# Kernel optimization log

Hardware: AMD Instinct MI355X
Metric: run time of the kernel (lower is better)

## Reference

```python
import jax, jax.numpy as jnp
import numpy as np

ATTR_LEN = [2, 4, 4, 2, 6]
CUM = np.concatenate(([0], np.cumsum(ATTR_LEN)))  # [0,2,6,10,12,18]
B, S, D, V = 4096, 200, 64, 100000


def setup_inputs() -> dict:
    key = jax.random.key(0)
    ks = jax.random.split(key, 10)
    x = jax.random.randint(ks[0], (B, S), 0, V)
    # one-hot labels per attribute, concatenated -> [B, 18]
    y_parts = []
    for i, al in enumerate(ATTR_LEN):
        lab = jax.random.randint(jax.random.fold_in(ks[1], i), (B,), 0, al)
        y_parts.append(jax.nn.one_hot(lab, al, dtype=jnp.float32))
    y = jnp.concatenate(y_parts, axis=1)
    emb_table = jax.random.normal(ks[2], (V, D), jnp.float32) * 0.02
    emb_table = emb_table.at[0].set(0.0)  # padding_idx=0
    att_w = jax.random.normal(ks[3], (5, D), jnp.float32) * 0.1
    att_b = jax.random.normal(ks[4], (5,), jnp.float32) * 0.1
    W0 = jax.random.normal(ks[5], (ATTR_LEN[0], D), jnp.float32) * 0.1
    W1 = jax.random.normal(ks[6], (ATTR_LEN[1], D), jnp.float32) * 0.1
    W2 = jax.random.normal(ks[7], (ATTR_LEN[2], D), jnp.float32) * 0.1
    W3 = jax.random.normal(ks[8], (ATTR_LEN[3], D), jnp.float32) * 0.1
    W4 = jax.random.normal(ks[9], (ATTR_LEN[4], D), jnp.float32) * 0.1
    return {"x": x, "y": y, "emb_table": emb_table, "att_w": att_w,
            "att_b": att_b, "W0": W0, "W1": W1, "W2": W2, "W3": W3, "W4": W4}


def reference(x, y, emb_table, att_w, att_b, W0, W1, W2, W3, W4):
    embed = emb_table[x]  # [B, S, D] gather (padding row is zero)
    # 5 per-attribute additive tanh-attention heads, batched over k.
    # Softmax over seq axis is independent per head, so stacking is exact.
    att_u = jnp.tanh(jnp.einsum('bsd,kd->bsk', embed, att_w) + att_b)  # [B,S,5]
    score = jax.nn.softmax(att_u, axis=1)                              # [B,S,5]
    user_rep = jnp.einsum('bsd,bsk->bkd', embed, score)                # [B,5,D]
    Ws = [W0, W1, W2, W3, W4]
    # per-task bias-free linear heads, concatenated -> [B, 18]
    W_user = jnp.concatenate([user_rep[:, i] @ Ws[i].T for i in range(5)], axis=1)
    logits = []
    loss = jnp.float32(0.0)
    for i in range(5):
        Wc = W_user[:, CUM[i]:CUM[i + 1]]
        yc = y[:, CUM[i]:CUM[i + 1]]
        # partial_training=False -> ob = ones -> all rows kept;
        # obj = exp(sum(W*y)) / sum_j exp(W_j)  ==  softmax picked at label
        logp = jax.nn.log_softmax(Wc, axis=1)
        loss = loss + (-jnp.sum(logp * yc) / Wc.shape[0])
        logits.append(jax.nn.softmax(Wc, axis=1))
    logit = jnp.concatenate(logits, axis=1)  # [B, 18]
    return logit, loss
```

## Files before the change

### kernel.cpp

```cpp
#include <hip/hip_runtime.h>
#include <math.h>

#define Bsz 4096
#define Ssz 200
#define Dsz 64
#define NK  5
#define NT  512
#define ROWH 72

typedef _Float16 half_t;
typedef _Float16 h2 __attribute__((ext_vector_type(2)));

__device__ inline h2 shfl_xor_h2(h2 v, int m) {
    int iv = __builtin_bit_cast(int, v);
    iv = __shfl_xor(iv, m);
    return __builtin_bit_cast(h2, iv);
}

__device__ inline h2 pk(float a, float b) {
    return __builtin_bit_cast(h2, __builtin_amdgcn_cvt_pkrtz(a, b));
}

__device__ inline float fdot2(h2 a, h2 b, float c) {
#if __has_builtin(__builtin_amdgcn_fdot2)
    return __builtin_amdgcn_fdot2(a, b, c, false);
#else
    return c + (float)a.x * (float)b.x + (float)a.y * (float)b.y;
#endif
}

__device__ inline float fast_tanh(float x) {
    float e = __expf(-2.0f * fabsf(x));
    float r = (1.0f - e) / (1.0f + e);
    return copysignf(r, x);
}

__global__ void zero_loss_kernel(float* loss) {
    if (threadIdx.x == 0) *loss = 0.0f;
}

__global__ __launch_bounds__(NT, 8) void tan_kernel(
    const int* __restrict__ x, const float* __restrict__ y,
    const float* __restrict__ emb_table,
    const float* __restrict__ att_w, const float* __restrict__ att_b,
    const float* __restrict__ W0, const float* __restrict__ W1,
    const float* __restrict__ W2, const float* __restrict__ W3,
    const float* __restrict__ W4,
    float* __restrict__ out_logit, float* __restrict__ loss_out)
{
    __shared__ alignas(16) half_t embh[Ssz * ROWH];
    __shared__ alignas(16) char   ovl[8 * NK * Dsz * 2];
    __shared__ alignas(16) h2     att5[100][8];
    __shared__ alignas(16) float  ur[NK][Dsz];
    __shared__ alignas(16) h2     awh[NK * 32];
    __shared__ alignas(16) int    xs[Ssz];
    __shared__ float wu[18];

    float*  att  = (float*)ovl;
    half_t (*urph)[NK][Dsz] = (half_t(*)[NK][Dsz])ovl;

    const int b   = blockIdx.x;
    const int tid = threadIdx.x;
    const int w   = tid >> 6;
    const int l   = tid & 63;

    if (tid < Ssz) xs[tid] = x[b * Ssz + tid];
    if (tid >= 256 && tid < 256 + NK * 32) {
        const int t = tid - 256;
        awh[t] = (h2){(half_t)att_w[2 * t], (half_t)att_w[2 * t + 1]};
    }
    __syncthreads();

    {
        float4 v[7];
#pragma unroll
        for (int p = 0; p < 7; ++p) {
            int i = tid + NT * p;
            if (i > Ssz * 16 - 1) i = Ssz * 16 - 1;
            const int s = i >> 4, c = i & 15;
            v[p] = ((const float4*)(emb_table + (size_t)xs[s] * Dsz))[c];
        }
#pragma unroll
        for (int p = 0; p < 7; ++p) {
            const int i = tid + NT * p;
            if (p < 6 || i < Ssz * 16) {
                const int s = i >> 4, c = i & 15;
                h2 lo = pk(v[p].x, v[p].y);
                h2 hi = pk(v[p].z, v[p].w);
                uint2 u = { __builtin_bit_cast(unsigned, lo),
                            __builtin_bit_cast(unsigned, hi) };
                *(uint2*)(embh + s * ROWH + c * 4) = u;
            }
        }
    }
    __syncthreads();

    if (tid < 2 * Ssz) {
        const int s = tid >> 1, h = tid & 1;
        union { uint4 q[4]; h2 hh[16]; } ue;
        const uint4* rp = (const uint4*)(embh + s * ROWH + h * 32);
#pragma unroll
        for (int i = 0; i < 4; ++i) ue.q[i] = rp[i];
        float acc[NK];
#pragma unroll 1
        for (int k = 0; k < NK; ++k) {
            union { uint4 q[4]; h2 hh[16]; } ua;
            const uint4* ap = (const uint4*)(awh + k * 32 + h * 16);
#pragma unroll
            for (int i = 0; i < 4; ++i) ua.q[i] = ap[i];
            float a = 0.f;
#pragma unroll
            for (int i = 0; i < 16; ++i) a = fdot2(ue.hh[i], ua.hh[i], a);
            acc[k] = a;
        }
#pragma unroll
        for (int k = 0; k < NK; ++k) acc[k] += __shfl_xor(acc[k], 1);
        if (h == 0) {
#pragma unroll
            for (int k = 0; k < NK; ++k)
                att[k * Ssz + s] = fast_tanh(acc[k] + att_b[k]);
        }
    }
    __syncthreads();

    if (w < NK) {
        const int k = w;
        float vals[4];
        float mx = -1e30f;
#pragma unroll
        for (int j = 0; j < 4; ++j) {
            int s = l + 64 * j;
            vals[j] = (s < Ssz) ? att[k * Ssz + s] : -1e30f;
            mx = fmaxf(mx, vals[j]);
        }
#pragma unroll
        for (int m = 32; m >= 1; m >>= 1) mx = fmaxf(mx, __shfl_xor(mx, m));
        float sum = 0.f;
#pragma unroll
        for (int j = 0; j < 4; ++j) {
            vals[j] = __expf(vals[j] - mx);
            sum += vals[j];
        }
#pragma unroll
        for (int m = 32; m >= 1; m >>= 1) sum += __shfl_xor(sum, m);
        float inv = 1.0f / sum;
#pragma unroll
        for (int j = 0; j < 4; ++j) {
            const int s = l + 64 * j;
            float scv = vals[j] * inv;
            float pnr = __shfl_xor(scv, 1);
            if (s < Ssz && (l & 1) == 0)
                att5[s >> 1][k] = pk(scv, pnr);
        }
    }
    __syncthreads();

    {
        const int c = tid & 15;
        const int j = tid >> 4;
        h2 acc[NK][2];
#pragma unroll
        for (int k = 0; k < NK; ++k) {
            acc[k][0] = (h2){(half_t)0, (half_t)0};
            acc[k][1] = (h2){(half_t)0, (half_t)0};
        }
#pragma unroll
        for (int t = 0; t < 4; ++t) {
            const int p = j + 32 * t;
            if (p < 100) {
                const int s0 = 2 * p;
                union { uint2 q; h2 hh[2]; } e0, e1;
                e0.q = *(const uint2*)(embh + s0 * ROWH + c * 4);
                e1.q = *(const uint2*)(embh + (s0 + 1) * ROWH + c * 4);
                union { uint4 q; h2 hh[4]; } sq;
                sq.q = *(const uint4*)(&att5[p][0]);
                h2 s4 = att5[p][4];
#pragma unroll
                for (int k = 0; k < NK; ++k) {
                    h2 sp = (k < 4) ? sq.hh[k] : s4;
                    h2 sc0 = (h2){sp.x, sp.x};
                    h2 sc1 = (h2){sp.y, sp.y};
                    acc[k][0] += e0.hh[0] * sc0;
                    acc[k][1] += e0.hh[1] * sc0;
                    acc[k][0] += e1.hh[0] * sc1;
                    acc[k][1] += e1.hh[1] * sc1;
                }
            }
        }
#pragma unroll
        for (int k = 0; k < NK; ++k)
#pragma unroll
            for (int i = 0; i < 2; ++i) {
                acc[k][i] += shfl_xor_h2(acc[k][i], 16);
                acc[k][i] += shfl_xor_h2(acc[k][i], 32);
            }
        if (l < 16) {
#pragma unroll
            for (int k = 0; k < NK; ++k) {
                union { h2 a[2]; uint2 q; } uu;
                uu.a[0] = acc[k][0]; uu.a[1] = acc[k][1];
                *(uint2*)(&urph[w][k][l * 4]) = uu.q;
            }
        }
    }
    __syncthreads();

    if (tid < NK * Dsz) {
        const int k = tid >> 6, d = tid & 63;
        float ssum = 0.f;
#pragma unroll
        for (int jj = 0; jj < 8; ++jj) ssum += (float)urph[jj][k][d];
        ur[k][d] = ssum;
    }
    __syncthreads();

    for (int j = w; j < 18; j += 8) {
        const float* Wp; int g, c0;
        if      (j < 2)  { g = 0; c0 = 0;  Wp = W0; }
        else if (j < 6)  { g = 1; c0 = 2;  Wp = W1; }
        else if (j < 10) { g = 2; c0 = 6;  Wp = W2; }
        else if (j < 12) { g = 3; c0 = 10; Wp = W3; }
        else             { g = 4; c0 = 12; Wp = W4; }
        float p = ur[g][l] * Wp[(j - c0) * Dsz + l];
#pragma unroll
        for (int m = 32; m >= 1; m >>= 1) p += __shfl_xor(p, m);
        if (l == 0) wu[j] = p;
    }
    __syncthreads();

    if (w == 0) {
        float lossb = 0.f;
        if (l < NK) {
            const int LEN[5] = {2, 4, 4, 2, 6};
            const int C0[5]  = {0, 2, 6, 10, 12};
            const int g = l, c0 = C0[g], len = LEN[g];
            float* op = out_logit + (size_t)b * 18;
            const float* yp = y + (size_t)b * 18;
            float mx = -1e30f;
            for (int j = 0; j < len; ++j) mx = fmaxf(mx, wu[c0 + j]);
            float sum = 0.f;
            for (int j = 0; j < len; ++j) sum += __expf(wu[c0 + j] - mx);
            float inv = 1.0f / sum;
            float lse = mx + __logf(sum);
            for (int j = 0; j < len; ++j) {
                op[c0 + j] = __expf(wu[c0 + j] - mx) * inv;
                lossb += (lse - wu[c0 + j]) * yp[c0 + j];
            }
        }
#pragma unroll
        for (int m = 1; m <= 4; m <<= 1) lossb += __shfl_xor(lossb, m);
        if (l == 0) atomicAdd(loss_out, lossb * (1.0f / Bsz));
    }
}

extern "C" void kernel_launch(void* const* d_in, const int* in_sizes, int n_in,
                              void* d_out, int out_size, void* d_ws, size_t ws_size,
                              hipStream_t stream) {
    const int*   x   = (const int*)d_in[0];
    const float* y   = (const float*)d_in[1];
    const float* emb = (const float*)d_in[2];
    const float* aw  = (const float*)d_in[3];
    const float* ab  = (const float*)d_in[4];
    const float* W0  = (const float*)d_in[5];
    const float* W1  = (const float*)d_in[6];
    const float* W2  = (const float*)d_in[7];
    const float* W3  = (const float*)d_in[8];
    const float* W4  = (const float*)d_in[9];
    float* out  = (float*)d_out;
    float* loss = out + (size_t)Bsz * 18;

    zero_loss_kernel<<<1, 64, 0, stream>>>(loss);
    tan_kernel<<<Bsz, NT, 0, stream>>>(x, y, emb, aw, ab,
                                       W0, W1, W2, W3, W4, out, loss);
}
```

Measured before the change: 151.5 us.

## Use MFMA for attention scores and weighted pooling with transposed embedding copy

Replaces the scalar fdot2 score computation and the packed-half weighted-sum pooling with 16x16x32 f16 MFMA instructions. A second, transposed copy of the embeddings is written to shared memory so the pooling MFMA reads contiguous sequence-major fragments. Scores are stored as padded half arrays, and the pooled result is reduced across two wave halves in fp32. This raises shared-memory use and lowers the launch-bounds occupancy hint from 8 to 4, and the scattered scalar transposed stores may cause bank conflicts. Most MFMA lanes are wasted because only 5 heads are computed.

```diff
diff --git a/kernel.cpp b/kernel.cpp
--- a/kernel.cpp
+++ b/kernel.cpp
@@ -1,32 +1,23 @@
 #include <hip/hip_runtime.h>
 #include <math.h>
+#include <stdint.h>
 
 #define Bsz 4096
 #define Ssz 200
 #define Dsz 64
 #define NK  5
 #define NT  512
-#define ROWH 72
 
 typedef _Float16 half_t;
-typedef _Float16 h2 __attribute__((ext_vector_type(2)));
-
-__device__ inline h2 shfl_xor_h2(h2 v, int m) {
-    int iv = __builtin_bit_cast(int, v);
-    iv = __shfl_xor(iv, m);
-    return __builtin_bit_cast(h2, iv);
-}
+typedef _Float16 h2    __attribute__((ext_vector_type(2)));
+typedef _Float16 f16x8 __attribute__((ext_vector_type(8)));
+typedef float    f32x4 __attribute__((ext_vector_type(4)));
+
+#define RSTRIDE 72
+#define TSTRIDE 232
 
 __device__ inline h2 pk(float a, float b) {
     return __builtin_bit_cast(h2, __builtin_amdgcn_cvt_pkrtz(a, b));
-}
-
-__device__ inline float fdot2(h2 a, h2 b, float c) {
-#if __has_builtin(__builtin_amdgcn_fdot2)
-    return __builtin_amdgcn_fdot2(a, b, c, false);
-#else
-    return c + (float)a.x * (float)b.x + (float)a.y * (float)b.y;
-#endif
 }
 
 __device__ inline float fast_tanh(float x) {
@@ -39,7 +30,7 @@
     if (threadIdx.x == 0) *loss = 0.0f;
 }
 
-__global__ __launch_bounds__(NT, 8) void tan_kernel(
+__global__ __launch_bounds__(NT, 4) void tan_kernel(
     const int* __restrict__ x, const float* __restrict__ y,
     const float* __restrict__ emb_table,
     const float* __restrict__ att_w, const float* __restrict__ att_b,
@@ -48,26 +39,38 @@
     const float* __restrict__ W4,
     float* __restrict__ out_logit, float* __restrict__ loss_out)
 {
-    __shared__ alignas(16) half_t embh[Ssz * ROWH];
-    __shared__ alignas(16) char   ovl[8 * NK * Dsz * 2];
-    __shared__ alignas(16) h2     att5[100][8];
-    __shared__ alignas(16) float  ur[NK][Dsz];
-    __shared__ alignas(16) h2     awh[NK * 32];
+    __shared__ alignas(16) half_t embR[208 * RSTRIDE];
+    __shared__ alignas(16) half_t embT[64 * TSTRIDE];
+    __shared__ alignas(16) float  ovl[1000];
+    __shared__ alignas(16) half_t ascore[NK * 240];
+    __shared__ alignas(16) half_t awh[NK * RSTRIDE];
     __shared__ alignas(16) int    xs[Ssz];
     __shared__ float wu[18];
 
-    float*  att  = (float*)ovl;
-    half_t (*urph)[NK][Dsz] = (half_t(*)[NK][Dsz])ovl;
+    float* att_raw = ovl;
 
     const int b   = blockIdx.x;
     const int tid = threadIdx.x;
     const int w   = tid >> 6;
     const int l   = tid & 63;
+    const int col = l & 15;
+    const int kg  = l >> 4;
 
     if (tid < Ssz) xs[tid] = x[b * Ssz + tid];
+    {
+        uint4 z = {0u, 0u, 0u, 0u};
+        if (tid < 72)
+            *(uint4*)((char*)embR + 200 * 144 + tid * 16) = z;
+        if (tid >= 72 && tid < 72 + 192) {
+            const int idx = tid - 72, row = idx / 3, q = idx - row * 3;
+            *(uint4*)((char*)embT + row * 464 + 400 + q * 16) = z;
+        }
+    }
     if (tid >= 256 && tid < 256 + NK * 32) {
-        const int t = tid - 256;
-        awh[t] = (h2){(half_t)att_w[2 * t], (half_t)att_w[2 * t + 1]};
+        const int t = tid - 256, row = t >> 5, cp = t & 31;
+        h2 v = {(half_t)att_w[row * 64 + 2 * cp],
+                (half_t)att_w[row * 64 + 2 * cp + 1]};
+        *(h2*)(awh + row * RSTRIDE + 2 * cp) = v;
     }
     __syncthreads();
 
@@ -89,36 +92,36 @@
                 h2 hi = pk(v[p].z, v[p].w);
                 uint2 u = { __builtin_bit_cast(unsigned, lo),
                             __builtin_bit_cast(unsigned, hi) };
-                *(uint2*)(embh + s * ROWH + c * 4) = u;
+                *(uint2*)(embR + s * RSTRIDE + c * 4) = u;
+                embT[(4 * c + 0) * TSTRIDE + s] = lo.x;
+                embT[(4 * c + 1) * TSTRIDE + s] = lo.y;
+                embT[(4 * c + 2) * TSTRIDE + s] = hi.x;
+                embT[(4 * c + 3) * TSTRIDE + s] = hi.y;
             }
         }
     }
     __syncthreads();
 
-    if (tid < 2 * Ssz) {
-        const int s = tid >> 1, h = tid & 1;
-        union { uint4 q[4]; h2 hh[16]; } ue;
-        const uint4* rp = (const uint4*)(embh + s * ROWH + h * 32);
-#pragma unroll
-        for (int i = 0; i < 4; ++i) ue.q[i] = rp[i];
-        float acc[NK];
-#pragma unroll 1
-        for (int k = 0; k < NK; ++k) {
-            union { uint4 q[4]; h2 hh[16]; } ua;
-            const uint4* ap = (const uint4*)(awh + k * 32 + h * 16);
-#pragma unroll
-            for (int i = 0; i < 4; ++i) ua.q[i] = ap[i];
-            float a = 0.f;
-#pragma unroll
-            for (int i = 0; i < 16; ++i) a = fdot2(ue.hh[i], ua.hh[i], a);
-            acc[k] = a;
-        }
-#pragma unroll
-        for (int k = 0; k < NK; ++k) acc[k] += __shfl_xor(acc[k], 1);
-        if (h == 0) {
-#pragma unroll
-            for (int k = 0; k < NK; ++k)
-                att[k * Ssz + s] = fast_tanh(acc[k] + att_b[k]);
+    {
+        const int brow = (col < 5) ? col : 0;
+        const f16x8 bw0 = *(const f16x8*)(awh + brow * RSTRIDE + kg * 8);
+        const f16x8 bw1 = *(const f16x8*)(awh + brow * RSTRIDE + 32 + kg * 8);
+        const float bk = att_b[brow];
+        for (int t = w; t < 13; t += 8) {
+            const int s = 16 * t + col;
+            const f16x8 a0 = *(const f16x8*)(embR + s * RSTRIDE + kg * 8);
+            const f16x8 a1 = *(const f16x8*)(embR + s * RSTRIDE + 32 + kg * 8);
+            f32x4 acc = {0.f, 0.f, 0.f, 0.f};
+            acc = __builtin_amdgcn_mfma_f32_16x16x32_f16(a0, bw0, acc, 0, 0, 0);
+            acc = __builtin_amdgcn_mfma_f32_16x16x32_f16(a1, bw1, acc, 0, 0, 0);
+            if (col < 5) {
+#pragma unroll
+                for (int r = 0; r < 4; ++r) {
+                    const int srow = 16 * t + 4 * kg + r;
+                    if (srow < Ssz)
+                        att_raw[col * 200 + srow] = fast_tanh(acc[r] + bk);
+                }
+            }
         }
     }
     __syncthreads();
@@ -129,8 +132,8 @@
         float mx = -1e30f;
 #pragma unroll
         for (int j = 0; j < 4; ++j) {
-            int s = l + 64 * j;
-            vals[j] = (s < Ssz) ? att[k * Ssz + s] : -1e30f;
+            const int s = l + 64 * j;
+            vals[j] = (s < Ssz) ? att_raw[k * 200 + s] : -1e30f;
             mx = fmaxf(mx, vals[j]);
         }
 #pragma unroll
@@ -143,85 +146,49 @@
         }
 #pragma unroll
         for (int m = 32; m >= 1; m >>= 1) sum += __shfl_xor(sum, m);
-        float inv = 1.0f / sum;
+        const float inv = 1.0f / sum;
 #pragma unroll
         for (int j = 0; j < 4; ++j) {
             const int s = l + 64 * j;
-            float scv = vals[j] * inv;
-            float pnr = __shfl_xor(scv, 1);
-            if (s < Ssz && (l & 1) == 0)
-                att5[s >> 1][k] = pk(scv, pnr);
-        }
-    }
-    __syncthreads();
-
-    {
-        const int c = tid & 15;
-        const int j = tid >> 4;
-        h2 acc[NK][2];
-#pragma unroll
-        for (int k = 0; k < NK; ++k) {
-            acc[k][0] = (h2){(half_t)0, (half_t)0};
-            acc[k][1] = (h2){(half_t)0, (half_t)0};
-        }
-#pragma unroll
-        for (int t = 0; t < 4; ++t) {
-            const int p = j + 32 * t;
-            if (p < 100) {
-                const int s0 = 2 * p;
-                union { uint2 q; h2 hh[2]; } e0, e1;
-                e0.q = *(const uint2*)(embh + s0 * ROWH + c * 4);
-                e1.q = *(const uint2*)(embh + (s0 + 1) * ROWH + c * 4);
-                union { uint4 q; h2 hh[4]; } sq;
-                sq.q = *(const uint4*)(&att5[p][0]);
-                h2 s4 = att5[p][4];
-#pragma unroll
-                for (int k = 0; k < NK; ++k) {
-                    h2 sp = (k < 4) ? sq.hh[k] : s4;
-                    h2 sc0 = (h2){sp.x, sp.x};
-                    h2 sc1 = (h2){sp.y, sp.y};
-                    acc[k][0] += e0.hh[0] * sc0;
-                    acc[k][1] += e0.hh[1] * sc0;
-                    acc[k][0] += e1.hh[0] * sc1;
-                    acc[k][1] += e1.hh[1] * sc1;
-                }
-            }
-        }
-#pragma unroll
-        for (int k = 0; k < NK; ++k)
-#pragma unroll
-            for (int i = 0; i < 2; ++i) {
-                acc[k][i] += shfl_xor_h2(acc[k][i], 16);
-                acc[k][i] += shfl_xor_h2(acc[k][i], 32);
-            }
-        if (l < 16) {
-#pragma unroll
-            for (int k = 0; k < NK; ++k) {
-                union { h2 a[2]; uint2 q; } uu;
-                uu.a[0] = acc[k][0]; uu.a[1] = acc[k][1];
-                *(uint2*)(&urph[w][k][l * 4]) = uu.q;
-            }
-        }
-    }
-    __syncthreads();
-
-    if (tid < NK * Dsz) {
-        const int k = tid >> 6, d = tid & 63;
-        float ssum = 0.f;
-#pragma unroll
-        for (int jj = 0; jj < 8; ++jj) ssum += (float)urph[jj][k][d];
-        ur[k][d] = ssum;
-    }
+            if (s < Ssz)      ascore[k * 240 + s] = (half_t)(vals[j] * inv);
+            else if (s < 224) ascore[k * 240 + s] = (half_t)0.0f;
+        }
+    }
+    __syncthreads();
+
+    {
+        const int dtile = w & 3, hh = w >> 2;
+        const int arow = (col < 5) ? col : 0;
+        const int KK0 = hh ? 4 : 0;
+        const int NKK = hh ? 3 : 4;
+        f32x4 acc = {0.f, 0.f, 0.f, 0.f};
+        for (int q = 0; q < NKK; ++q) {
+            const int kk = KK0 + q;
+            const f16x8 af = *(const f16x8*)(embT + (dtile * 16 + col) * TSTRIDE
+                                             + kk * 32 + kg * 8);
+            const f16x8 bf = *(const f16x8*)(ascore + arow * 240 + kk * 32 + kg * 8);
+            acc = __builtin_amdgcn_mfma_f32_16x16x32_f16(af, bf, acc, 0, 0, 0);
+        }
+        float* urp = ovl + hh * 320;
+        if (col < 5) {
+#pragma unroll
+            for (int r = 0; r < 4; ++r)
+                urp[col * 64 + dtile * 16 + 4 * kg + r] = acc[r];
+        }
+    }
+    __syncthreads();
+
+    if (tid < NK * Dsz) ovl[640 + tid] = ovl[tid] + ovl[320 + tid];
     __syncthreads();
 
     for (int j = w; j < 18; j += 8) {
-        const float* Wp; int g, c0;
-        if      (j < 2)  { g = 0; c0 = 0;  Wp = W0; }
-        else if (j < 6)  { g = 1; c0 = 2;  Wp = W1; }
-        else if (j < 10) { g = 2; c0 = 6;  Wp = W2; }
-        else if (j < 12) { g = 3; c0 = 10; Wp = W3; }
-        else             { g = 4; c0 = 12; Wp = W4; }
-        float p = ur[g][l] * Wp[(j - c0) * Dsz + l];
+        const float* Wp; int gr, c0;
+        if      (j < 2)  { gr = 0; c0 = 0;  Wp = W0; }
+        else if (j < 6)  { gr = 1; c0 = 2;  Wp = W1; }
+        else if (j < 10) { gr = 2; c0 = 6;  Wp = W2; }
+        else if (j < 12) { gr = 3; c0 = 10; Wp = W3; }
+        else             { gr = 4; c0 = 12; Wp = W4; }
+        float p = ovl[640 + gr * 64 + l] * Wp[(j - c0) * Dsz + l];
 #pragma unroll
         for (int m = 32; m >= 1; m >>= 1) p += __shfl_xor(p, m);
         if (l == 0) wu[j] = p;
@@ -233,7 +200,7 @@
         if (l < NK) {
             const int LEN[5] = {2, 4, 4, 2, 6};
             const int C0[5]  = {0, 2, 6, 10, 12};
-            const int g = l, c0 = C0[g], len = LEN[g];
+            const int gidx = l, c0 = C0[gidx], len = LEN[gidx];
             float* op = out_logit + (size_t)b * 18;
             const float* yp = y + (size_t)b * 18;
             float mx = -1e30f;
```

Measured after the change: 167.7 us. 1.11x slower.
